# Kernel tuning notes

Hardware: AMD Instinct MI355X
Metric: run time of the kernel (lower is better)

Reference implementation:

```python
import jax, jax.numpy as jnp
import numpy as np

IN_FEATURES = 4096
OUT_FEATURES = 11008
GROUP_SIZE = 128
NUM_GROUPS = IN_FEATURES // GROUP_SIZE  # 32


def setup_inputs() -> dict:
    key = jax.random.key(0)
    k1, k2, k3, k4, k5 = jax.random.split(key, 5)
    x = jax.random.normal(k1, (4, 2048, IN_FEATURES), dtype=jnp.float32)
    # packed 4-bit weights: each int holds (high << 4) | low, values in [0, 256)
    qweight = jax.random.randint(k2, (IN_FEATURES // 2, OUT_FEATURES), 0, 256, dtype=jnp.int32)
    scales = jax.random.uniform(k3, (NUM_GROUPS, OUT_FEATURES), dtype=jnp.float32) * 0.01 + 1e-4
    zeros = jax.random.normal(k4, (NUM_GROUPS, OUT_FEATURES), dtype=jnp.float32) * 0.01
    bias = jax.random.normal(k5, (OUT_FEATURES,), dtype=jnp.float32) * 0.01
    return {"x": x, "qweight": qweight, "scales": scales, "zeros": zeros, "bias": bias}


def _dequantize(qweight, scales, zeros, dtype):
    # unpack two 4-bit values per byte; even input rows = low nibble, odd = high nibble
    low = ((qweight & 15) - 8).astype(dtype)          # [in/2, out]
    high = (((qweight >> 4) & 15) - 8).astype(dtype)  # [in/2, out]
    w = jnp.stack([low, high], axis=1).reshape(IN_FEATURES, OUT_FEATURES)
    # per-group affine dequant: w = q * scale + zero
    w = w.reshape(NUM_GROUPS, GROUP_SIZE, OUT_FEATURES)
    w = w * scales[:, None, :] + zeros[:, None, :]
    return w.reshape(IN_FEATURES, OUT_FEATURES)


def reference(x, qweight, scales, zeros, bias):
    weight = _dequantize(qweight, scales, zeros, x.dtype)  # [in, out]
    # F.linear(x, weight.T, bias) == x @ weight + bias
    return jnp.einsum('bsi,io->bso', x, weight) + bias
```

## Files before the change

### kernel.cpp

```cpp
#include <hip/hip_runtime.h>
#include <hip/hip_bf16.h>

#define IN_F 4096
#define OUT_F 11008
#define GSIZE 128
#define M_TOTAL 8192

typedef float f32x4 __attribute__((ext_vector_type(4)));
typedef float f32x16 __attribute__((ext_vector_type(16)));
typedef unsigned short u16x8 __attribute__((ext_vector_type(8)));
typedef unsigned int u32x4 __attribute__((ext_vector_type(4)));
typedef __bf16 bf16x8 __attribute__((ext_vector_type(8)));

#define ASG __attribute__((address_space(1)))
#define ASL __attribute__((address_space(3)))

__device__ __forceinline__ unsigned short f2bf(float f) {
    union { float f; unsigned int u; } v;
    v.f = f;
    unsigned int u = v.u;
    unsigned int r = (u + 0x7fffu + ((u >> 16) & 1u)) >> 16;
    return (unsigned short)r;
}


__global__ void convert_x_frag_kernel(const float* __restrict__ x,
                                      unsigned short* __restrict__ xb) {
    const int mf = blockIdx.x;
    const int r  = threadIdx.x >> 3;
    const int kb = (threadIdx.x & 7) * 8;
    const int k0 = blockIdx.y * 512;
    const float* src = x + (size_t)(mf * 32 + r) * IN_F;
    unsigned short* dst = xb + (size_t)mf * (IN_F / 16) * 512;
#pragma unroll
    for (int kk = 0; kk < 512; kk += 64) {
        const int k = k0 + kk + kb;
        f32x4 a = *(const f32x4*)(src + k);
        f32x4 b = *(const f32x4*)(src + k + 4);
        u16x8 v;
#pragma unroll
        for (int e = 0; e < 4; ++e) {
            v[e]     = f2bf(a[e]);
            v[e + 4] = f2bf(b[e]);
        }
        const int kf = k >> 4, q2 = (k >> 3) & 1;
        *(u16x8*)(dst + (size_t)kf * 512 + (q2 * 32 + r) * 8) = v;
    }
}

__global__ void dequant_w_frag_kernel(const int* __restrict__ qw,
                                      const float* __restrict__ scales,
                                      const float* __restrict__ zeros,
                                      unsigned short* __restrict__ wt) {
    const int n  = blockIdx.x * 256 + threadIdx.x;
    const int k0 = blockIdx.y * 32;
    const int g  = k0 >> 7;
    const float s = scales[(size_t)g * OUT_F + n];
    const float z = zeros[(size_t)g * OUT_F + n];

    unsigned short outv[32];
#pragma unroll
    for (int i = 0; i < 16; ++i) {
        int q = qw[(size_t)(k0 / 2 + i) * OUT_F + n];
        float lo = (float)((q & 15) - 8) * s + z;
        float hi = (float)(((q >> 4) & 15) - 8) * s + z;
        outv[2 * i]     = f2bf(lo);
        outv[2 * i + 1] = f2bf(hi);
    }
    const int nf = n >> 5, r32 = n & 31;
    unsigned short* base = wt + (size_t)nf * (IN_F / 16) * 512 +
                           (size_t)(k0 >> 4) * 512;
    const u16x8* sv = (const u16x8*)outv;
#pragma unroll
    for (int c = 0; c < 4; ++c)
        *(u16x8*)(base + (c >> 1) * 512 + ((c & 1) * 32 + r32) * 8) = sv[c];
}

__global__ void dequant_w_rowmajor_kernel(const int* __restrict__ qw,
                                          const float* __restrict__ scales,
                                          const float* __restrict__ zeros,
                                          unsigned short* __restrict__ wt) {
    const int n  = blockIdx.x * 256 + threadIdx.x;
    const int k0 = blockIdx.y * 32;
    const int g  = k0 >> 7;
    const float s = scales[(size_t)g * OUT_F + n];
    const float z = zeros[(size_t)g * OUT_F + n];

    unsigned short outv[32];
#pragma unroll
    for (int i = 0; i < 16; ++i) {
        int q = qw[(size_t)(k0 / 2 + i) * OUT_F + n];
        float lo = (float)((q & 15) - 8) * s + z;
        float hi = (float)(((q >> 4) & 15) - 8) * s + z;
        outv[2 * i]     = f2bf(lo);
        outv[2 * i + 1] = f2bf(hi);
    }
    u16x8* dst = (u16x8*)(wt + (size_t)n * IN_F + k0);
    const u16x8* src = (const u16x8*)outv;
#pragma unroll
    for (int i = 0; i < 4; ++i) dst[i] = src[i];
}

__global__ __launch_bounds__(512, 1)
void gemm_8phase(const unsigned short* __restrict__ xb,
                 const unsigned short* __restrict__ wt,
                 const float* __restrict__ bias,
                 float* __restrict__ out) {
    constexpr int NT = IN_F / 64;
    constexpr int NKF = IN_F / 16;
    __shared__ __attribute__((aligned(128))) unsigned short lds[65536];

    const int bid = (int)blockIdx.x;
    const int xcd = bid & 7;
    const int l   = bid >> 3;
    const int m0 = (xcd * 4 + (l & 3)) * 256;
    const int n0 = (l >> 2) * 256;

    const int tid  = threadIdx.x;
    const int lane = tid & 63;
    const int wave = tid >> 6;
    const int wr = wave >> 2;
    const int wc = wave & 3;
    const int r32 = lane & 31;
    const int q2  = lane >> 5;

    const ASG char* xbc = (const ASG char*)xb;
    const ASG char* wtc = (const ASG char*)wt;
    ASL char* ldsc = (ASL char*)lds;

    const int mfb = m0 >> 5;
    const int nfb = n0 >> 5;
    unsigned int oA[4], oB[4];
    int dA[4], dB[4];
#pragma unroll
    for (int H = 0; H < 2; ++H)
#pragma unroll
        for (int i = 0; i < 2; ++i) {
            const int s = i * 8 + wave;
            const int rf = s >> 2, kc = s & 3;
            oA[H * 2 + i] = (unsigned int)(((mfb + H * 4 + rf) * NKF + kc) * 1024 +
                                           lane * 16);
            dA[H * 2 + i] = (H * 16 + s) * 1024;
        }
#pragma unroll
    for (int G = 0; G < 2; ++G)
#pragma unroll
        for (int i = 0; i < 2; ++i) {
            const int s = i * 8 + wave;
            const int cf = (s >> 2) * 2 + G, kc = s & 3;
            oB[G * 2 + i] = (unsigned int)(((nfb + cf) * NKF + kc) * 1024 +
                                           lane * 16);
            dB[G * 2 + i] = 32768 + (cf * 4 + kc) * 1024;
        }

#define STG_A(H, P)                                                            \
    do {                                                                       \
        _Pragma("unroll") for (int _i = 0; _i < 2; ++_i)                       \
            __builtin_amdgcn_global_load_lds(                                  \
                (ASG const unsigned int*)(xbc + oA[(H) * 2 + _i]),             \
                (ASL unsigned int*)(ldsc + dA[(H) * 2 + _i] + (P) * 65536),    \
                16, 0, 0);                                                     \
    } while (0)
#define STG_BG(G, P)                                                           \
    do {                                                                       \
        _Pragma("unroll") for (int _i = 0; _i < 2; ++_i)                       \
            __builtin_amdgcn_global_load_lds(                                  \
                (ASG const unsigned int*)(wtc + oB[(G) * 2 + _i]),             \
                (ASL unsigned int*)(ldsc + dB[(G) * 2 + _i] + (P) * 65536),    \
                16, 0, 0);                                                     \
    } while (0)
#define ADV_A(H) do { oA[(H)*2] += 4096; oA[(H)*2+1] += 4096; } while (0)
#define ADV_BG(G) do { oB[(G)*2] += 4096; oB[(G)*2+1] += 4096; } while (0)

#define BAR()                                                                  \
    do {                                                                       \
        __builtin_amdgcn_sched_barrier(0);                                     \
        __builtin_amdgcn_s_barrier();                                          \
        __builtin_amdgcn_sched_barrier(0);                                     \
    } while (0)

    bf16x8 afH0[2][4], afH1[2][4];
    bf16x8 bfE[4], bfO[4];
    f32x16 acc[4][2];
#pragma unroll
    for (int i = 0; i < 4; ++i)
#pragma unroll
        for (int j = 0; j < 2; ++j) acc[i][j] = (f32x16)0.0f;

#define READ_A0(P)                                                             \
    do {                                                                       \
        const unsigned short* _ab = lds + (P) * 32768 + lane * 8;              \
        _Pragma("unroll") for (int _m = 0; _m < 2; ++_m)                       \
        _Pragma("unroll") for (int _kc = 0; _kc < 4; ++_kc)                    \
            afH0[_m][_kc] = *(const bf16x8*)(_ab +                             \
                (((wr * 4 + _m) * 4 + _kc) << 9));                             \
    } while (0)
#define READ_A1(P)                                                             \
    do {                                                                       \
        const unsigned short* _ab = lds + (P) * 32768 + lane * 8;              \
        _Pragma("unroll") for (int _m = 0; _m < 2; ++_m)                       \
        _Pragma("unroll") for (int _kc = 0; _kc < 4; ++_kc)                    \
            afH1[_m][_kc] = *(const bf16x8*)(_ab +                             \
                (((wr * 4 + 2 + _m) * 4 + _kc) << 9));                         \
    } while (0)
#define READ_BLO(P)                                                            \
    do {                                                                       \
        const unsigned short* _bb = lds + (P) * 32768 + 16384 + lane * 8;      \
        _Pragma("unroll") for (int _kc = 0; _kc < 4; ++_kc)                    \
            bfE[_kc] = *(const bf16x8*)(_bb +                                  \
                (((wc * 2) * 4 + _kc) << 9));                                  \
    } while (0)
#define READ_BHI(P)                                                            \
    do {                                                                       \
        const unsigned short* _bb = lds + (P) * 32768 + 16384 + lane * 8;      \
        _Pragma("unroll") for (int _kc = 0; _kc < 4; ++_kc)                    \
            bfO[_kc] = *(const bf16x8*)(_bb +                                  \
                (((wc * 2 + 1) * 4 + _kc) << 9));                              \
    } while (0)

#define QUADX(AF, BF, MH, NH)                                                  \
    do {                                                                       \
        __builtin_amdgcn_s_setprio(1);                                         \
        _Pragma("unroll") for (int _m = 0; _m < 2; ++_m)                       \
        _Pragma("unroll") for (int _kc = 0; _kc < 4; ++_kc)                    \
            acc[(MH) * 2 + _m][(NH)] =                                         \
                __builtin_amdgcn_mfma_f32_32x32x16_bf16(                       \
                    AF[_m][_kc], BF[_kc], acc[(MH) * 2 + _m][(NH)], 0, 0, 0);  \
        __builtin_amdgcn_s_setprio(0);                                         \
    } while (0)

    STG_BG(0, 0); ADV_BG(0);
    STG_BG(1, 0); ADV_BG(1);
    STG_A(0, 0);  ADV_A(0);
    STG_A(1, 0);  ADV_A(1);
    STG_BG(0, 1); ADV_BG(0);
    STG_BG(1, 1); ADV_BG(1);
    STG_A(0, 1);  ADV_A(0);
    __builtin_amdgcn_sched_barrier(0);
    asm volatile("s_waitcnt vmcnt(6)" ::: "memory");
    BAR();

#pragma unroll 1
    for (int tt = 0; tt < NT; tt += 2) {
        const bool g2 = (tt + 2 < NT);
        const bool g3 = (tt + 3 < NT);
        READ_A0(0);
        READ_BLO(0);
        STG_A(1, 1); ADV_A(1);
        BAR();
        QUADX(afH0, bfE, 0, 0);
        READ_BHI(0);
        if (g2) STG_BG(0, 0);
        ADV_BG(0);
        BAR();
        QUADX(afH0, bfO, 0, 1);
        READ_A1(0);
        if (g2) STG_BG(1, 0);
        ADV_BG(1);
        BAR();
        QUADX(afH1, bfE, 1, 0);
        if (g2) STG_A(0, 0);
        ADV_A(0);
        __builtin_amdgcn_sched_barrier(0);
        if (tt < NT - 2) {
            asm volatile("s_waitcnt vmcnt(6)" ::: "memory");
        } else {
            asm volatile("s_waitcnt vmcnt(0)" ::: "memory");
        }
        BAR();
        QUADX(afH1, bfO, 1, 1);
        READ_A0(1);
        READ_BLO(1);
        if (g2) STG_A(1, 0);
        ADV_A(1);
        BAR();
        QUADX(afH0, bfE, 0, 0);
        READ_BHI(1);
        if (g3) STG_BG(0, 1);
        ADV_BG(0);
        BAR();
        QUADX(afH0, bfO, 0, 1);
        READ_A1(1);
        if (g3) STG_BG(1, 1);
        ADV_BG(1);
        BAR();
        QUADX(afH1, bfE, 1, 0);
        if (g3) STG_A(0, 1);
        ADV_A(0);
        __builtin_amdgcn_sched_barrier(0);
        if (tt + 1 < NT - 2) {
            asm volatile("s_waitcnt vmcnt(6)" ::: "memory");
        } else {
            asm volatile("s_waitcnt vmcnt(0)" ::: "memory");
        }
        BAR();
        QUADX(afH1, bfO, 1, 1);
    }

#pragma unroll
    for (int nf = 0; nf < 2; ++nf) {
        const int col = n0 + wc * 64 + nf * 32 + r32;
        const float bv = bias[col];
#pragma unroll
        for (int mf = 0; mf < 4; ++mf) {
            const int row0 = m0 + wr * 128 + mf * 32 + q2 * 4;
#pragma unroll
            for (int r = 0; r < 16; ++r) {
                const int row = row0 + (r & 3) + ((r >> 2) << 3);
                __builtin_nontemporal_store(acc[mf][nf][r] + bv,
                                            &out[(size_t)row * OUT_F + col]);
            }
        }
    }
#undef STG_A
#undef STG_BG
#undef ADV_A
#undef ADV_BG
#undef BAR
#undef READ_A0
#undef READ_A1
#undef READ_BLO
#undef READ_BHI
#undef QUADX
}

template <bool PREW>
__global__ __launch_bounds__(256, 2)
void gemm_kernel(const float* __restrict__ x,
                 const unsigned short* __restrict__ wt,
                 const int* __restrict__ qw,
                 const float* __restrict__ scales,
                 const float* __restrict__ zeros,
                 const float* __restrict__ bias,
                 float* __restrict__ out) {
    constexpr int BM = 128, BN = 128, BK = 64;
    constexpr int LDK = BK + 8;
    constexpr int NT = IN_F / BK;

    __shared__ unsigned short As[BM * LDK];
    __shared__ unsigned short Bs[BN * LDK];

    const int bid = blockIdx.x;
    constexpr int NB_N = OUT_F / BN;
    const int m0 = (bid / NB_N) * BM;
    const int n0 = (bid % NB_N) * BN;

    const int tid  = threadIdx.x;
    const int lane = tid & 63;
    const int wave = tid >> 6;
    const int wr = wave >> 1, wc = wave & 1;

    const int st_row = tid >> 3;
    const int st_col = (tid & 7) * 8;

    f32x4 areg[4][2];
    u32x4 breg[4];
    int   qreg[16];
    float s_, z_;
    const int b_n  = tid & 127;
    const int b_kp = (tid >> 7) * 16;

    auto load_tile = [&](int kt) {
        {
            const float* base = x + (size_t)m0 * IN_F + (size_t)kt * BK + st_col;
#pragma unroll
            for (int p = 0; p < 4; ++p) {
                const float* rp = base + (size_t)(p * 32 + st_row) * IN_F;
                areg[p][0] = *(const f32x4*)rp;
                areg[p][1] = *(const f32x4*)(rp + 4);
            }
        }
        if constexpr (PREW) {
            const unsigned short* base = wt + (size_t)n0 * IN_F + (size_t)kt * BK + st_col;
#pragma unroll
            for (int p = 0; p < 4; ++p)
                breg[p] = *(const u32x4*)(base + (size_t)(p * 32 + st_row) * IN_F);
        } else {
            const int kp0 = kt * (BK / 2) + b_kp;
#pragma unroll
            for (int i = 0; i < 16; ++i)
                qreg[i] = qw[(size_t)(kp0 + i) * OUT_F + n0 + b_n];
            const int g = (kt * BK) >> 7;
            s_ = scales[(size_t)g * OUT_F + n0 + b_n];
            z_ = zeros[(size_t)g * OUT_F + n0 + b_n];
        }
    };

    auto write_lds = [&]() {
#pragma unroll
        for (int p = 0; p < 4; ++p) {
            u16x8 v;
#pragma unroll
            for (int e = 0; e < 4; ++e) {
                v[e]     = f2bf(areg[p][0][e]);
                v[e + 4] = f2bf(areg[p][1][e]);
            }
            *(u16x8*)(&As[(p * 32 + st_row) * LDK + st_col]) = v;
        }
        if constexpr (PREW) {
#pragma unroll
            for (int p = 0; p < 4; ++p)
                *(u32x4*)(&Bs[(p * 32 + st_row) * LDK + st_col]) = breg[p];
        } else {
            unsigned short tmp[32];
#pragma unroll
            for (int i = 0; i < 16; ++i) {
                int q = qreg[i];
                tmp[2 * i]     = f2bf((float)((q & 15) - 8) * s_ + z_);
                tmp[2 * i + 1] = f2bf((float)(((q >> 4) & 15) - 8) * s_ + z_);
            }
            const u16x8* srcv = (const u16x8*)tmp;
#pragma unroll
            for (int i = 0; i < 4; ++i)
                *(u16x8*)(&Bs[b_n * LDK + 2 * b_kp + 8 * i]) = srcv[i];
        }
    };

    f32x4 acc[4][4];
#pragma unroll
    for (int i = 0; i < 4; ++i)
#pragma unroll
        for (int j = 0; j < 4; ++j) acc[i][j] = (f32x4)0.0f;

    load_tile(0);

#pragma unroll 1
    for (int kt = 0; kt < NT; ++kt) {
        __syncthreads();
        write_lds();
        __syncthreads();
        if (kt + 1 < NT) load_tile(kt + 1);

#pragma unroll
        for (int kk = 0; kk < 2; ++kk) {
            const int kidx = kk * 32 + ((lane >> 4) << 3);
            bf16x8 afv[4], bfv[4];
#pragma unroll
            for (int i = 0; i < 4; ++i)
                afv[i] = *(const bf16x8*)(&As[(wr * 64 + i * 16 + (lane & 15)) * LDK + kidx]);
#pragma unroll
            for (int j = 0; j < 4; ++j)
                bfv[j] = *(const bf16x8*)(&Bs[(wc * 64 + j * 16 + (lane & 15)) * LDK + kidx]);
#pragma unroll
            for (int i = 0; i < 4; ++i)
#pragma unroll
                for (int j = 0; j < 4; ++j)
                    acc[i][j] = __builtin_amdgcn_mfma_f32_16x16x32_bf16(afv[i], bfv[j], acc[i][j], 0, 0, 0);
        }
    }

    const int orow_base = m0 + wr * 64 + ((lane >> 4) << 2);
    const int ocol_base = n0 + wc * 64 + (lane & 15);
#pragma unroll
    for (int j = 0; j < 4; ++j) {
        const float bv = bias[ocol_base + j * 16];
#pragma unroll
        for (int i = 0; i < 4; ++i) {
#pragma unroll
            for (int q = 0; q < 4; ++q) {
                out[(size_t)(orow_base + i * 16 + q) * OUT_F + (ocol_base + j * 16)] =
                    acc[i][j][q] + bv;
            }
        }
    }
}

extern "C" void kernel_launch(void* const* d_in, const int* in_sizes, int n_in,
                              void* d_out, int out_size, void* d_ws, size_t ws_size,
                              hipStream_t stream) {
    const float* x      = (const float*)d_in[0];
    const int*   qw     = (const int*)d_in[1];
    const float* scales = (const float*)d_in[2];
    const float* zeros  = (const float*)d_in[3];
    const float* bias   = (const float*)d_in[4];
    float* out = (float*)d_out;

    const size_t wt_bytes = (size_t)OUT_F * IN_F * sizeof(unsigned short);
    const size_t xb_bytes = (size_t)M_TOTAL * IN_F * sizeof(unsigned short);

    if (ws_size >= wt_bytes + xb_bytes) {
        unsigned short* wt = (unsigned short*)d_ws;
        unsigned short* xb = (unsigned short*)((char*)d_ws + wt_bytes);
        convert_x_frag_kernel<<<dim3(M_TOTAL / 32, 8), 256, 0, stream>>>(x, xb);
        dequant_w_frag_kernel<<<dim3(OUT_F / 256, IN_F / 32), 256, 0, stream>>>(qw, scales, zeros, wt);
        gemm_8phase<<<(M_TOTAL / 256) * (OUT_F / 256), 512, 0, stream>>>(xb, wt, bias, out);
    } else if (ws_size >= wt_bytes) {
        unsigned short* wt = (unsigned short*)d_ws;
        dequant_w_rowmajor_kernel<<<dim3(OUT_F / 256, IN_F / 32), 256, 0, stream>>>(qw, scales, zeros, wt);
        gemm_kernel<true><<<(M_TOTAL / 128) * (OUT_F / 128), 256, 0, stream>>>(x, wt, qw, scales, zeros, bias, out);
    } else {
        gemm_kernel<false><<<(M_TOTAL / 128) * (OUT_F / 128), 256, 0, stream>>>(x, nullptr, qw, scales, zeros, bias, out);
    }
}
```

Measured before the change: 702.9 us.

## Restructure GEMM main loop into k-chunk phases with register double-buffering

Replaces the 8-phase quadrant schedule (A/B halves staged and read separately) with a k-chunk schedule. Each of 4 phases per tile stages one 16-wide k slice of both A and B, reads the next slice's fragments into an alternate register set, and issues 8 MFMAs over the full 4x2 accumulator block. This aims for a more regular overlap of LDS reads and global-to-LDS loads with MFMA work. The cost is a different barrier and vmcnt pattern. The LDS reads for the next tile now wait behind the vmcnt drain, which could expose latency.

```diff
diff --git a/kernel.cpp b/kernel.cpp
--- a/kernel.cpp
+++ b/kernel.cpp
@@ -102,10 +102,10 @@
 }
 
 __global__ __launch_bounds__(512, 1)
-void gemm_8phase(const unsigned short* __restrict__ xb,
-                 const unsigned short* __restrict__ wt,
-                 const float* __restrict__ bias,
-                 float* __restrict__ out) {
+void gemm_kc(const unsigned short* __restrict__ xb,
+             const unsigned short* __restrict__ wt,
+             const float* __restrict__ bias,
+             float* __restrict__ out) {
     constexpr int NT = IN_F / 64;
     constexpr int NKF = IN_F / 16;
     __shared__ __attribute__((aligned(128))) unsigned short lds[65536];
@@ -133,44 +133,24 @@
     unsigned int oA[4], oB[4];
     int dA[4], dB[4];
 #pragma unroll
-    for (int H = 0; H < 2; ++H)
-#pragma unroll
-        for (int i = 0; i < 2; ++i) {
-            const int s = i * 8 + wave;
-            const int rf = s >> 2, kc = s & 3;
-            oA[H * 2 + i] = (unsigned int)(((mfb + H * 4 + rf) * NKF + kc) * 1024 +
-                                           lane * 16);
-            dA[H * 2 + i] = (H * 16 + s) * 1024;
-        }
-#pragma unroll
-    for (int G = 0; G < 2; ++G)
-#pragma unroll
-        for (int i = 0; i < 2; ++i) {
-            const int s = i * 8 + wave;
-            const int cf = (s >> 2) * 2 + G, kc = s & 3;
-            oB[G * 2 + i] = (unsigned int)(((nfb + cf) * NKF + kc) * 1024 +
-                                           lane * 16);
-            dB[G * 2 + i] = 32768 + (cf * 4 + kc) * 1024;
-        }
-
-#define STG_A(H, P)                                                            \
+    for (int kc = 0; kc < 4; ++kc) {
+        oA[kc] = (unsigned int)(((mfb + wave) * NKF + kc) * 1024 + lane * 16);
+        oB[kc] = (unsigned int)(((nfb + wave) * NKF + kc) * 1024 + lane * 16);
+        dA[kc] = (wave * 4 + kc) * 1024;
+        dB[kc] = 32768 + (wave * 4 + kc) * 1024;
+    }
+
+#define STG_Z(KC, P)                                                           \
     do {                                                                       \
-        _Pragma("unroll") for (int _i = 0; _i < 2; ++_i)                       \
-            __builtin_amdgcn_global_load_lds(                                  \
-                (ASG const unsigned int*)(xbc + oA[(H) * 2 + _i]),             \
-                (ASL unsigned int*)(ldsc + dA[(H) * 2 + _i] + (P) * 65536),    \
-                16, 0, 0);                                                     \
+        __builtin_amdgcn_global_load_lds(                                      \
+            (ASG const unsigned int*)(xbc + oA[(KC)]),                         \
+            (ASL unsigned int*)(ldsc + dA[(KC)] + (P) * 65536), 16, 0, 0);     \
+        __builtin_amdgcn_global_load_lds(                                      \
+            (ASG const unsigned int*)(wtc + oB[(KC)]),                         \
+            (ASL unsigned int*)(ldsc + dB[(KC)] + (P) * 65536), 16, 0, 0);     \
+        oA[(KC)] += 4096;                                                      \
+        oB[(KC)] += 4096;                                                      \
     } while (0)
-#define STG_BG(G, P)                                                           \
-    do {                                                                       \
-        _Pragma("unroll") for (int _i = 0; _i < 2; ++_i)                       \
-            __builtin_amdgcn_global_load_lds(                                  \
-                (ASG const unsigned int*)(wtc + oB[(G) * 2 + _i]),             \
-                (ASL unsigned int*)(ldsc + dB[(G) * 2 + _i] + (P) * 65536),    \
-                16, 0, 0);                                                     \
-    } while (0)
-#define ADV_A(H) do { oA[(H)*2] += 4096; oA[(H)*2+1] += 4096; } while (0)
-#define ADV_BG(G) do { oB[(G)*2] += 4096; oB[(G)*2+1] += 4096; } while (0)
 
 #define BAR()                                                                  \
     do {                                                                       \
@@ -179,122 +159,77 @@
         __builtin_amdgcn_sched_barrier(0);                                     \
     } while (0)
 
-    bf16x8 afH0[2][4], afH1[2][4];
-    bf16x8 bfE[4], bfO[4];
+    bf16x8 afR[2][4];
+    bf16x8 bfR[2][2];
     f32x16 acc[4][2];
 #pragma unroll
     for (int i = 0; i < 4; ++i)
 #pragma unroll
         for (int j = 0; j < 2; ++j) acc[i][j] = (f32x16)0.0f;
 
-#define READ_A0(P)                                                             \
+#define READ_KC(P, KC, S)                                                      \
     do {                                                                       \
-        const unsigned short* _ab = lds + (P) * 32768 + lane * 8;              \
-        _Pragma("unroll") for (int _m = 0; _m < 2; ++_m)                       \
-        _Pragma("unroll") for (int _kc = 0; _kc < 4; ++_kc)                    \
-            afH0[_m][_kc] = *(const bf16x8*)(_ab +                             \
-                (((wr * 4 + _m) * 4 + _kc) << 9));                             \
+        const unsigned short* _b = lds + (P) * 32768 + lane * 8;               \
+        _Pragma("unroll") for (int _m = 0; _m < 4; ++_m)                       \
+            afR[S][_m] = *(const bf16x8*)(_b +                                 \
+                (((wr * 4 + _m) * 4 + (KC)) << 9));                            \
+        _Pragma("unroll") for (int _n = 0; _n < 2; ++_n)                       \
+            bfR[S][_n] = *(const bf16x8*)(_b + 16384 +                         \
+                (((wc * 2 + _n) * 4 + (KC)) << 9));                            \
     } while (0)
-#define READ_A1(P)                                                             \
-    do {                                                                       \
-        const unsigned short* _ab = lds + (P) * 32768 + lane * 8;              \
-        _Pragma("unroll") for (int _m = 0; _m < 2; ++_m)                       \
-        _Pragma("unroll") for (int _kc = 0; _kc < 4; ++_kc)                    \
-            afH1[_m][_kc] = *(const bf16x8*)(_ab +                             \
-                (((wr * 4 + 2 + _m) * 4 + _kc) << 9));                         \
-    } while (0)
-#define READ_BLO(P)                                                            \
-    do {                                                                       \
-        const unsigned short* _bb = lds + (P) * 32768 + 16384 + lane * 8;      \
-        _Pragma("unroll") for (int _kc = 0; _kc < 4; ++_kc)                    \
-            bfE[_kc] = *(const bf16x8*)(_bb +                                  \
-                (((wc * 2) * 4 + _kc) << 9));                                  \
-    } while (0)
-#define READ_BHI(P)                                                            \
-    do {                                                                       \
-        const unsigned short* _bb = lds + (P) * 32768 + 16384 + lane * 8;      \
-        _Pragma("unroll") for (int _kc = 0; _kc < 4; ++_kc)                    \
-            bfO[_kc] = *(const bf16x8*)(_bb +                                  \
-                (((wc * 2 + 1) * 4 + _kc) << 9));                              \
-    } while (0)
-
-#define QUADX(AF, BF, MH, NH)                                                  \
+
+#define QUAD_KC(S)                                                             \
     do {                                                                       \
         __builtin_amdgcn_s_setprio(1);                                         \
-        _Pragma("unroll") for (int _m = 0; _m < 2; ++_m)                       \
-        _Pragma("unroll") for (int _kc = 0; _kc < 4; ++_kc)                    \
-            acc[(MH) * 2 + _m][(NH)] =                                         \
-                __builtin_amdgcn_mfma_f32_32x32x16_bf16(                       \
-                    AF[_m][_kc], BF[_kc], acc[(MH) * 2 + _m][(NH)], 0, 0, 0);  \
+        _Pragma("unroll") for (int _m = 0; _m < 4; ++_m)                       \
+        _Pragma("unroll") for (int _n = 0; _n < 2; ++_n)                       \
+            acc[_m][_n] = __builtin_amdgcn_mfma_f32_32x32x16_bf16(             \
+                afR[S][_m], bfR[S][_n], acc[_m][_n], 0, 0, 0);                 \
         __builtin_amdgcn_s_setprio(0);                                         \
     } while (0)
 
-    STG_BG(0, 0); ADV_BG(0);
-    STG_BG(1, 0); ADV_BG(1);
-    STG_A(0, 0);  ADV_A(0);
-    STG_A(1, 0);  ADV_A(1);
-    STG_BG(0, 1); ADV_BG(0);
-    STG_BG(1, 1); ADV_BG(1);
-    STG_A(0, 1);  ADV_A(0);
+#pragma unroll
+    for (int kc = 0; kc < 4; ++kc) STG_Z(kc, 0);
+#pragma unroll
+    for (int kc = 0; kc < 4; ++kc) STG_Z(kc, 1);
     __builtin_amdgcn_sched_barrier(0);
-    asm volatile("s_waitcnt vmcnt(6)" ::: "memory");
+    asm volatile("s_waitcnt vmcnt(8)" ::: "memory");
+    BAR();
+    READ_KC(0, 0, 0);
     BAR();
 
 #pragma unroll 1
     for (int tt = 0; tt < NT; tt += 2) {
         const bool g2 = (tt + 2 < NT);
         const bool g3 = (tt + 3 < NT);
-        READ_A0(0);
-        READ_BLO(0);
-        STG_A(1, 1); ADV_A(1);
-        BAR();
-        QUADX(afH0, bfE, 0, 0);
-        READ_BHI(0);
-        if (g2) STG_BG(0, 0);
-        ADV_BG(0);
-        BAR();
-        QUADX(afH0, bfO, 0, 1);
-        READ_A1(0);
-        if (g2) STG_BG(1, 0);
-        ADV_BG(1);
-        BAR();
-        QUADX(afH1, bfE, 1, 0);
-        if (g2) STG_A(0, 0);
-        ADV_A(0);
+        QUAD_KC(0); READ_KC(0, 1, 1); if (g2) STG_Z(0, 0); BAR();
+        QUAD_KC(1); READ_KC(0, 2, 0); if (g2) STG_Z(1, 0); BAR();
+        QUAD_KC(0); READ_KC(0, 3, 1); if (g2) STG_Z(2, 0); BAR();
+        QUAD_KC(1);
+        if (g2) STG_Z(3, 0);
         __builtin_amdgcn_sched_barrier(0);
         if (tt < NT - 2) {
-            asm volatile("s_waitcnt vmcnt(6)" ::: "memory");
+            asm volatile("s_waitcnt vmcnt(8)" ::: "memory");
         } else {
             asm volatile("s_waitcnt vmcnt(0)" ::: "memory");
         }
+        __builtin_amdgcn_sched_barrier(0);
+        READ_KC(1, 0, 0);
         BAR();
-        QUADX(afH1, bfO, 1, 1);
-        READ_A0(1);
-        READ_BLO(1);
-        if (g2) STG_A(1, 0);
-        ADV_A(1);
-        BAR();
-        QUADX(afH0, bfE, 0, 0);
-        READ_BHI(1);
-        if (g3) STG_BG(0, 1);
-        ADV_BG(0);
-        BAR();
-        QUADX(afH0, bfO, 0, 1);
-        READ_A1(1);
-        if (g3) STG_BG(1, 1);
-        ADV_BG(1);
-        BAR();
-        QUADX(afH1, bfE, 1, 0);
-        if (g3) STG_A(0, 1);
-        ADV_A(0);
+        QUAD_KC(0); READ_KC(1, 1, 1); if (g3) STG_Z(0, 1); BAR();
+        QUAD_KC(1); READ_KC(1, 2, 0); if (g3) STG_Z(1, 1); BAR();
+        QUAD_KC(0); READ_KC(1, 3, 1); if (g3) STG_Z(2, 1); BAR();
+        QUAD_KC(1);
+        if (g3) STG_Z(3, 1);
         __builtin_amdgcn_sched_barrier(0);
         if (tt + 1 < NT - 2) {
-            asm volatile("s_waitcnt vmcnt(6)" ::: "memory");
+            asm volatile("s_waitcnt vmcnt(8)" ::: "memory");
         } else {
             asm volatile("s_waitcnt vmcnt(0)" ::: "memory");
         }
+        __builtin_amdgcn_sched_barrier(0);
+        if (g2) READ_KC(0, 0, 0);
         BAR();
-        QUADX(afH1, bfO, 1, 1);
     }
 
 #pragma unroll
@@ -312,16 +247,10 @@
             }
         }
     }
-#undef STG_A
-#undef STG_BG
-#undef ADV_A
-#undef ADV_BG
+#undef STG_Z
 #undef BAR
-#undef READ_A0
-#undef READ_A1
-#undef READ_BLO
-#undef READ_BHI
-#undef QUADX
+#undef READ_KC
+#undef QUAD_KC
 }
 
 template <bool PREW>
@@ -483,7 +412,7 @@
         unsigned short* xb = (unsigned short*)((char*)d_ws + wt_bytes);
         convert_x_frag_kernel<<<dim3(M_TOTAL / 32, 8), 256, 0, stream>>>(x, xb);
         dequant_w_frag_kernel<<<dim3(OUT_F / 256, IN_F / 32), 256, 0, stream>>>(qw, scales, zeros, wt);
-        gemm_8phase<<<(M_TOTAL / 256) * (OUT_F / 256), 512, 0, stream>>>(xb, wt, bias, out);
+        gemm_kc<<<(M_TOTAL / 256) * (OUT_F / 256), 512, 0, stream>>>(xb, wt, bias, out);
     } else if (ws_size >= wt_bytes) {
         unsigned short* wt = (unsigned short*)d_ws;
         dequant_w_rowmajor_kernel<<<dim3(OUT_F / 256, IN_F / 32), 256, 0, stream>>>(qw, scales, zeros, wt);
```

Result: no change. 689.8 us (-1.9%).
